# Optimization experiments

Measured on AMD Instinct MI355X. Metric: run time of the kernel, lower is better.

## Reference

```python
import jax, jax.numpy as jnp
import numpy as np
from jax import lax

P = 8       # patch_size
TEMP = 30.0 # softmax temperature from RelationUnit.temp


def _conv3x3(x, w, b, groups):
    # x: [B, C, H, W], w: [O, C//groups, 3, 3]
    y = lax.conv_general_dilated(x, w, (1, 1), 'SAME', feature_group_count=groups)
    return y + b[None, :, None, None]


def _unfold(x):
    # nn.Unfold(kernel=P, stride=P): [B,C,H,W] -> [B, C*P*P, n], channel-major then (ki,kj)
    B, C, H, W = x.shape
    x = x.reshape(B, C, H // P, P, W // P, P)
    x = x.transpose(0, 1, 3, 5, 2, 4)          # [B,C,P,P,H/P,W/P]
    return x.reshape(B, C * P * P, (H // P) * (W // P))


def _fold(x, H, W):
    # inverse of _unfold (non-overlapping patches)
    B, CPP, n = x.shape
    C = CPP // (P * P)
    x = x.reshape(B, C, P, P, H // P, W // P)
    x = x.transpose(0, 1, 4, 2, 5, 3)          # [B,C,H/P,P,W/P,P]
    return x.reshape(B, C, H, W)


def _head(query, key, value, wq, bq, wk, bk, wv, bv):
    # one RelationUnit (heads=1 internally)
    b, tq, c, h, w = query.shape
    t = key.shape[1]
    n = (h // P) * (w // P)
    d = P * P * c

    q = _conv3x3(query.reshape(-1, c, h, w), wq, bq, groups=c)   # depthwise
    k = _conv3x3(key.reshape(-1, c, h, w), wk, bk, groups=c)     # depthwise
    v = _conv3x3(value.reshape(-1, c, h, w), wv, bv, groups=1)   # dense

    # [b*t, d, n] -> [b, d, t*n]  (matches view/permute chain in torch code)
    uq = _unfold(q).reshape(b, tq, d, n).transpose(0, 2, 1, 3).reshape(b, d, tq * n)
    uk = _unfold(k).reshape(b, t, d, n).transpose(0, 2, 1, 3).reshape(b, d, t * n)
    uv = _unfold(v).reshape(b, t, d, n).transpose(0, 2, 1, 3).reshape(b, d, t * n)

    attn = jnp.einsum('bdq,bdk->bqk', uq, uk) * (d ** -0.5)
    attn = jax.nn.softmax(attn * TEMP, axis=-1)
    out = jnp.einsum('bqk,bdk->bqd', attn, uv)                   # [b, tq*n, d]

    out = out.reshape(b, tq, n, d).transpose(0, 1, 3, 2).reshape(b * tq, d, n)
    feat = _fold(out, h, w)                                      # [b*tq, c, h, w]
    return feat.reshape(query.shape)


def reference(query, key, value, Wq, bq, Wk, bk, Wv, bv):
    heads = jax.vmap(_head, in_axes=(None, None, None, 0, 0, 0, 0, 0, 0))(
        query, key, value, Wq, bq, Wk, bk, Wv, bv)               # [Nh, b, tq, c, h, w]
    Nh = heads.shape[0]
    return jnp.concatenate([heads[i] for i in range(Nh)], axis=-1)


def setup_inputs() -> dict:
    key = jax.random.key(0)
    ks = jax.random.split(key, 6)
    b, tq, t, c, h, w, Nh = 1, 2, 2, 32, 224, 336, 4
    f32 = jnp.float32
    rn = lambda k, s, sc=1.0: jax.random.normal(k, s, f32) * sc
    return {
        'query': rn(ks[0], (b, tq, c, h, w)),
        'key':   rn(ks[1], (b, t, c, h, w)),
        'value': rn(ks[2], (b, t, c, h, w)),
        'Wq': rn(ks[3], (Nh, c, 1, 3, 3), 0.1), 'bq': jnp.zeros((Nh, c), f32),
        'Wk': rn(ks[4], (Nh, c, 1, 3, 3), 0.1), 'bk': jnp.zeros((Nh, c), f32),
        'Wv': rn(ks[5], (Nh, c, c, 3, 3), 0.05), 'bv': jnp.zeros((Nh, c), f32),
    }
```

## Files before the change

kernel.cpp:

```cpp
#include <hip/hip_runtime.h>
#include <hip/hip_bf16.h>

#define T_FR 2
#define C_CH 32
#define H_IMG 224
#define W_IMG 336
#define NH 4
#define NPATCH 1176
#define NQ 2352
#define NPAD 2432
#define DD 2048
#define WOUT (W_IMG*NH)
#define SM_SCALE 0.6629126073623885f
#define PIX_F (H_IMG*W_IMG)
#define PIX_T (T_FR*PIX_F)

typedef __attribute__((ext_vector_type(4))) float f32x4;
typedef __attribute__((ext_vector_type(8))) short short8;
typedef unsigned short ushort_t;
typedef __attribute__((ext_vector_type(4))) unsigned short u16x4;
typedef __attribute__((ext_vector_type(8))) unsigned short u16x8;

__device__ inline ushort_t f2bf(float x){
  union { float f; unsigned int u; } v; v.f = x;
  unsigned int r = v.u + 0x7fffu + ((v.u >> 16) & 1u);
  return (ushort_t)(r >> 16);
}

__device__ inline void gload16(const void* g, void* l){
  __builtin_amdgcn_global_load_lds(
      (const __attribute__((address_space(1))) void*)g,
      (__attribute__((address_space(3))) void*)l,
      16, 0, 0);
}

__global__ __launch_bounds__(256) void zero_pads(
    ushort_t* __restrict__ Qu, ushort_t* __restrict__ Ku,
    ushort_t* __restrict__ Vu, int nh)
{
  const int per = 80*DD;
  int tot = 3*nh*per;
  for (int id = blockIdx.x*256 + threadIdx.x; id < tot; id += gridDim.x*256){
    int buf = id / (nh*per);
    int rem = id - buf*(nh*per);
    int h = rem / per;
    int e = rem - h*per;
    ushort_t* B = (buf==0) ? Qu : (buf==1) ? Ku : Vu;
    B[((size_t)h*NPAD + NQ)*DD + e] = 0;
  }
}

__global__ __launch_bounds__(256) void transpose_cl(
    const float* __restrict__ in, ushort_t* __restrict__ inCL)
{
  int id = blockIdx.x*256 + threadIdx.x;
  int t = id / PIX_F;
  int p = id - t*PIX_F;
  const float* src = in + (size_t)t*C_CH*PIX_F + p;
  #pragma unroll
  for (int oct=0; oct<4; oct++){
    u16x8 u;
    #pragma unroll
    for (int e=0; e<8; e++)
      u[e] = f2bf(src[(size_t)(oct*8+e)*PIX_F]);
    *(u16x8*)&inCL[(size_t)id*C_CH + oct*8] = u;
  }
}

__global__ __launch_bounds__(256) void prep_wb(
    const float* __restrict__ Wv, ushort_t* __restrict__ Wb)
{
  int idx = blockIdx.x*256 + threadIdx.x;
  if (idx >= 9*128*32) return;
  int tap = idx >> 12;
  int og  = (idx >> 5) & 127;
  int cc  = idx & 31;
  Wb[idx] = f2bf(Wv[(size_t)og*288 + cc*9 + tap]);
}

__global__ __launch_bounds__(256) void dwconv_unfold(
    const float* __restrict__ in, const float* __restrict__ Wd,
    const float* __restrict__ bd, ushort_t* __restrict__ outU,
    int head0, int nh)
{
  int id = blockIdx.x*256 + threadIdx.x;
  int cc = id & 31;
  int rest = id >> 5;
  int xseg = rest % 42;
  rest /= 42;
  int y = rest % H_IMG;
  int t = rest / H_IMG;

  const float* src = in + ((size_t)(t*C_CH + cc)*H_IMG)*W_IMG;
  int x0 = xseg*8;

  float r0[10], r1[10], r2[10];
  #pragma unroll
  for (int j=0;j<10;j++){
    int xx = x0 + j - 1;
    bool xok = (xx>=0) && (xx<W_IMG);
    r0[j] = (xok && y>0)         ? src[(size_t)(y-1)*W_IMG+xx] : 0.f;
    r1[j] = (xok)                ? src[(size_t)y*W_IMG+xx]     : 0.f;
    r2[j] = (xok && y<H_IMG-1)   ? src[(size_t)(y+1)*W_IMG+xx] : 0.f;
  }
  int qrow = t*NPATCH + (y>>3)*42 + xseg;
  int dcol = (y&7)*256 + cc*8;

  for (int h = 0; h < nh; ++h){
    const float* w = Wd + ((size_t)(head0+h)*C_CH + cc)*9;
    float w0=w[0],w1=w[1],w2=w[2],w3=w[3],w4=w[4],w5=w[5],w6=w[6],w7=w[7],w8=w[8];
    float bias = bd[(size_t)(head0+h)*C_CH + cc];
    u16x8 res;
    #pragma unroll
    for (int j=0;j<8;j++){
      float a = bias;
      a += r0[j]*w0 + r0[j+1]*w1 + r0[j+2]*w2;
      a += r1[j]*w3 + r1[j+1]*w4 + r1[j+2]*w5;
      a += r2[j]*w6 + r2[j+1]*w7 + r2[j+2]*w8;
      res[j] = f2bf(a);
    }
    *(u16x8*)&outU[((size_t)h*NPAD + qrow)*DD + dcol] = res;
  }
}

#define VA_HALO 0
#define VA_BS   37120
#define V_LDS   73984

__global__ __launch_bounds__(256) void vconv_mfma(
    const ushort_t* __restrict__ inCL, const ushort_t* __restrict__ Wb,
    const float* __restrict__ bvv, ushort_t* __restrict__ Vu, int head0)
{
  __shared__ __align__(16) char lds[V_LDS];
  int xt = blockIdx.x;
  int pr_g = blockIdx.y;
  int z  = blockIdx.z;
  int t  = pr_g / 28, pr = pr_g - t*28;
  int x0 = xt*56, y0 = pr*8;
  int tid = threadIdx.x, lane = tid & 63, wid = tid >> 6;

  for (int i = tid; i < 580; i += 256){
    int ly = i/58, lx = i - (i/58)*58;
    int gy = y0 - 1 + ly, gx = x0 - 1 + lx;
    u16x8 v0={},v1={},v2={},v3={};
    if (gy>=0 && gy<H_IMG && gx>=0 && gx<W_IMG){
      const u16x8* s = (const u16x8*)&inCL[((size_t)t*PIX_F + gy*W_IMG + gx)*C_CH];
      v0=s[0]; v1=s[1]; v2=s[2]; v3=s[3];
    }
    *(u16x8*)&lds[VA_HALO + 0*9280 + i*16] = v0;
    *(u16x8*)&lds[VA_HALO + 1*9280 + i*16] = v1;
    *(u16x8*)&lds[VA_HALO + 2*9280 + i*16] = v2;
    *(u16x8*)&lds[VA_HALO + 3*9280 + i*16] = v3;
  }
  for (int i = tid; i < 576; i += 256){
    int tap = i/64, ol = i - (i/64)*64;
    const u16x8* s = (const u16x8*)&Wb[((size_t)tap*128 + head0*32 + z*64 + ol)*C_CH];
    #pragma unroll
    for (int oct=0; oct<4; oct++)
      *(u16x8*)&lds[VA_BS + tap*4096 + ol*64 + ((oct^(ol&3))<<4)] = s[oct];
  }
  __syncthreads();

  int aoff[7];
  #pragma unroll
  for (int m=0;m<7;m++){
    int pm = wid*112 + m*16 + (lane&15);
    int yl = pm/56, xl = pm - yl*56;
    aoff[m] = VA_HALO + (lane>>4)*9280 + (yl*58 + xl)*16;
  }

  f32x4 acc[7][4] = {};
  #pragma unroll
  for (int tap=0; tap<9; tap++){
    const int dy = tap/3, dx = tap - (tap/3)*3;
    short8 bfr[4];
    #pragma unroll
    for (int n=0;n<4;n++){
      int ol = n*16 + (lane&15);
      bfr[n] = *(const short8*)&lds[VA_BS + tap*4096 + ol*64 + ((((lane>>4))^(ol&3))<<4)];
    }
    #pragma unroll
    for (int m=0;m<7;m++){
      short8 af = *(const short8*)&lds[aoff[m] + (dy*58+dx)*16];
      #pragma unroll
      for (int n=0;n<4;n++)
        acc[m][n] = __builtin_amdgcn_mfma_f32_16x16x32_bf16(af, bfr[n], acc[m][n], 0,0,0);
    }
  }
  __syncthreads();

  float bias[4];
  #pragma unroll
  for (int n=0;n<4;n++){
    int ol = n*16 + (lane&15);
    bias[n] = bvv[(size_t)(head0 + z*2 + (ol>>5))*C_CH + (ol&31)];
  }
  #pragma unroll
  for (int m=0;m<7;m++){
    #pragma unroll
    for (int j=0;j<4;j++){
      int p = wid*112 + m*16 + (lane>>4)*4 + j;
      int yl = p/56, xl = p - (p/56)*56;
      int kl = xl >> 3;
      int off = yl*8 + (xl&7);
      #pragma unroll
      for (int n=0;n<4;n++){
        int ol = n*16 + (lane&15);
        int addr = ((ol>>5)*7 + kl)*4096 + (off*32 + (ol&31))*2;
        *(ushort_t*)&lds[addr] = f2bf(acc[m][n][j] + bias[n]);
      }
    }
  }
  __syncthreads();
  int key0 = t*NPATCH + pr*42 + xt*7;
  #pragma unroll
  for (int i=0;i<14;i++){
    int c = i*256 + tid;
    int hib = c / 1792;
    int rem = c - hib*1792;
    int kl = rem >> 8, dch = rem & 255;
    u16x8 v = *(const u16x8*)&lds[c*16];
    *(u16x8*)&Vu[((size_t)(z*2+hib)*NPAD + key0 + kl)*DD + dch*8] = v;
  }
}

__global__ __launch_bounds__(256) void vtranspose(
    const ushort_t* __restrict__ Vu, ushort_t* __restrict__ Vt)
{
  __shared__ ushort_t tile[64*68];
  int d0 = blockIdx.x*64;
  int k0 = blockIdx.y*64;
  const ushort_t* src = Vu + (size_t)blockIdx.z*NPAD*DD;
  ushort_t* dst = Vt + (size_t)blockIdx.z*DD*NPAD;
  int t = threadIdx.x;
  #pragma unroll
  for (int i=0;i<2;i++){
    int key = (t>>3) + i*32;
    int dd  = (t&7)*8;
    u16x8 v = *(const u16x8*)&src[(size_t)(k0+key)*DD + d0+dd];
    #pragma unroll
    for (int e=0;e<8;e++) tile[(dd+e)*68 + key] = v[e];
  }
  __syncthreads();
  #pragma unroll
  for (int i=0;i<2;i++){
    int dd  = (t>>3) + i*32;
    int key = (t&7)*8;
    u16x4 a = *(const u16x4*)&tile[dd*68 + key];
    u16x4 b = *(const u16x4*)&tile[dd*68 + key + 4];
    u16x8 v;
    v[0]=a[0]; v[1]=a[1]; v[2]=a[2]; v[3]=a[3];
    v[4]=b[0]; v[5]=b[1]; v[6]=b[2]; v[7]=b[3];
    *(u16x8*)&dst[(size_t)(d0+dd)*NPAD + k0+key] = v;
  }
}

#define ABASE(b,kc) ((b)*32768 + (kc)*16384)
#define BBASE(b,kc) (65536 + (b)*32768 + (kc)*16384)

#define STG(dstb, Mat, t0, Rm1, ktc) { \
  int i0_ = tid;       int r0_ = i0_>>2; int c0_ = ((i0_&3) ^ ((r0_>>1)&3)); \
  gload16(Mat + (size_t)min(t0 + r0_, Rm1)*(size_t)K + (ktc) + c0_*8, \
          lds + (dstb) + (tid & ~63)*16); \
  int i1_ = 512 + tid; int r1_ = i1_>>2; int c1_ = ((i1_&3) ^ ((r1_>>1)&3)); \
  gload16(Mat + (size_t)min(t0 + r1_, Rm1)*(size_t)K + (ktc) + c1_*8, \
          lds + (dstb) + (512 + (tid & ~63))*16); }

#define RDAF(b,kc,mh) { _Pragma("unroll") \
  for (int m=0;m<4;m++) \
    af[m] = *(const short8*)(lds + ABASE(b,kc) + (wr*128 + (mh)*64 + m*16 + l15)*64 + rkB); }

#define RDBF(b,kc) { _Pragma("unroll") \
  for (int n=0;n<4;n++) \
    bf[n] = *(const short8*)(lds + BBASE(b,kc) + (wc*64 + n*16 + l15)*64 + rkB); }

#define LEADBAR() { __builtin_amdgcn_sched_barrier(0); \
  __builtin_amdgcn_s_barrier(); __builtin_amdgcn_sched_barrier(0); }

#define MFMA16(mh) { __builtin_amdgcn_s_setprio(1); \
  _Pragma("unroll") for (int m=0;m<4;m++){ \
    _Pragma("unroll") for (int n=0;n<4;n++) \
      acc[(mh)*4+m][n] = __builtin_amdgcn_mfma_f32_16x16x32_bf16(af[m], bf[n], acc[(mh)*4+m][n], 0,0,0); } \
  __builtin_amdgcn_s_setprio(0); }

#define TRAILBAR() { __builtin_amdgcn_sched_barrier(0); \
  __builtin_amdgcn_s_barrier(); __builtin_amdgcn_sched_barrier(0); }

#define GATEBAR(cond) { __builtin_amdgcn_sched_barrier(0); \
  if (cond) { asm volatile("s_waitcnt vmcnt(4)" ::: "memory"); } \
  else      { asm volatile("s_waitcnt vmcnt(0)" ::: "memory"); } \
  __builtin_amdgcn_s_barrier(); __builtin_amdgcn_sched_barrier(0); }

template<int MODE>
__global__ __launch_bounds__(512) void gemm8p(
    const ushort_t* __restrict__ A, const ushort_t* __restrict__ B,
    float* __restrict__ C, float* __restrict__ Out,
    int K, int Am1, int Bm1, size_t aStr, size_t bStr, int head0)
{
  __shared__ __align__(16) char lds[131072];
  int tid = threadIdx.x, lane = tid & 63, wid = tid >> 6;

  int gx = gridDim.x, gy = gridDim.y;
  int nwg = gx*gy*gridDim.z;
  int id  = (blockIdx.z*gy + blockIdx.y)*gx + blockIdx.x;
  int swz = (id & 7)*(nwg >> 3) + (id >> 3);
  int bx = swz % gx; int tmp = swz / gx;
  int by = tmp % gy; int bz = tmp / gy;

  const ushort_t* Ab = A + (size_t)bz*aStr;
  const ushort_t* Bb = B + (size_t)bz*bStr;
  int row0 = by*256, col0 = bx*256;
  int wr = wid >> 2, wc = wid & 3;
  int l15 = lane & 15;
  int rkB = (((lane>>4) ^ ((l15>>1)&3)) * 16);

  f32x4 acc[8][4] = {};
  int NT = K >> 6;
  int NI = NT >> 1;

  STG(ABASE(0,0), Ab, row0, Am1, 0)
  STG(BBASE(0,0), Bb, col0, Bm1, 0)
  STG(ABASE(0,1), Ab, row0, Am1, 32)
  STG(BBASE(0,1), Bb, col0, Bm1, 32)
  STG(ABASE(1,0), Ab, row0, Am1, 64)
  STG(BBASE(1,0), Bb, col0, Bm1, 64)
  __builtin_amdgcn_sched_barrier(0);
  asm volatile("s_waitcnt vmcnt(4)" ::: "memory");
  __builtin_amdgcn_s_barrier();
  __builtin_amdgcn_sched_barrier(0);

  #pragma unroll 1
  for (int it = 0; it < NI; ++it){
    int T1k = (2*it+1) << 6;
    int T2k = (2*it+2) << 6;
    int T3k = (2*it+3) << 6;
    bool s2 = (2*it+2 < NT), s3 = (2*it+3 < NT);
    short8 af[4], bf[4];

    RDAF(0,0,0) RDBF(0,0)
    STG(ABASE(1,1), Ab, row0, Am1, T1k+32)
    LEADBAR() MFMA16(0) TRAILBAR()
    RDAF(0,0,1)
    STG(BBASE(1,1), Bb, col0, Bm1, T1k+32)
    LEADBAR() MFMA16(1) TRAILBAR()
    RDAF(0,1,0) RDBF(0,1)
    if (s2) STG(ABASE(0,0), Ab, row0, Am1, T2k)
    LEADBAR() MFMA16(0) TRAILBAR()
    RDAF(0,1,1)
    if (s2) STG(BBASE(0,0), Bb, col0, Bm1, T2k)
    LEADBAR() MFMA16(1)
    GATEBAR(s2)
    RDAF(1,0,0) RDBF(1,0)
    if (s2) STG(ABASE(0,1), Ab, row0, Am1, T2k+32)
    LEADBAR() MFMA16(0) TRAILBAR()
    RDAF(1,0,1)
    if (s2) STG(BBASE(0,1), Bb, col0, Bm1, T2k+32)
    LEADBAR() MFMA16(1) TRAILBAR()
    RDAF(1,1,0) RDBF(1,1)
    if (s3) STG(ABASE(1,0), Ab, row0, Am1, T3k)
    LEADBAR() MFMA16(0) TRAILBAR()
    RDAF(1,1,1)
    if (s3) STG(BBASE(1,0), Bb, col0, Bm1, T3k)
    LEADBAR() MFMA16(1)
    GATEBAR(s3)
  }

  int rb0 = row0 + wr*128 + (lane>>4)*4;
  int cb0 = col0 + wc*64 + l15;
  if (MODE == 0){
    float* Cb = C + (size_t)bz*NPAD*(size_t)NPAD;
    #pragma unroll
    for (int M=0;M<8;M++)
      #pragma unroll
      for (int n=0;n<4;n++){
        int col = cb0 + n*16;
        if (col < NPAD)
          #pragma unroll
          for (int j=0;j<4;j++){
            int row = rb0 + M*16 + j;
            if (row < NPAD)
              Cb[(size_t)row*NPAD + col] = acc[M][n][j];
          }
      }
  } else {
    int head = head0 + bz;
    #pragma unroll
    for (int M=0;M<8;M++){
      #pragma unroll
      for (int j=0;j<4;j++){
        int q = rb0 + M*16 + j;
        if (q < NQ){
          int t = q / NPATCH;
          int p = q - t*NPATCH;
          int hi = p / 42, wi = p - hi*42;
          #pragma unroll
          for (int n=0;n<4;n++){
            int dd = cb0 + n*16;
            int cch = dd & 31;
            int off = dd >> 5;
            int pi = off >> 3, pj = off & 7;
            int yy = hi*8 + pi, xx = wi*8 + pj;
            Out[(((size_t)t*C_CH + cch)*H_IMG + yy)*WOUT + (size_t)head*W_IMG + xx]
              = acc[M][n][j];
          }
        }
      }
    }
  }
}

__global__ __launch_bounds__(256) void softmax_rows(
    const float* __restrict__ S, ushort_t* __restrict__ Pm)
{
  const float* row = S + ((size_t)blockIdx.y*NPAD + blockIdx.x)*NPAD;
  ushort_t* prow = Pm + ((size_t)blockIdx.y*NPAD + blockIdx.x)*NPAD;
  int tid = threadIdx.x;
  __shared__ float red[4];

  float mx = -3.0e38f;
  #pragma unroll
  for (int i=0;i<10;i++){
    int k = tid + i*256;
    if (k < NQ) mx = fmaxf(mx, row[k]);
  }
  #pragma unroll
  for (int o=32;o;o>>=1) mx = fmaxf(mx, __shfl_xor(mx, o));
  if ((tid&63)==0) red[tid>>6] = mx;
  __syncthreads();
  mx = fmaxf(fmaxf(red[0],red[1]), fmaxf(red[2],red[3]));
  __syncthreads();

  float e[10]; float s = 0.f;
  #pragma unroll
  for (int i=0;i<10;i++){
    int k = tid + i*256;
    float v = 0.f;
    if (k < NQ) v = __expf((row[k]-mx)*SM_SCALE);
    e[i] = v; s += v;
  }
  #pragma unroll
  for (int o=32;o;o>>=1) s += __shfl_xor(s, o);
  if ((tid&63)==0) red[tid>>6] = s;
  __syncthreads();
  s = (red[0]+red[1]) + (red[2]+red[3]);
  float inv = 1.0f / s;
  #pragma unroll
  for (int i=0;i<10;i++){
    int k = tid + i*256;
    if (k < NQ) prow[k] = f2bf(e[i]*inv);
  }
  if (tid < NPAD-NQ) prow[NQ+tid] = 0;
}

extern "C" void kernel_launch(void* const* d_in, const int* in_sizes, int n_in,
                              void* d_out, int out_size, void* d_ws, size_t ws_size,
                              hipStream_t stream)
{
  const float* query = (const float*)d_in[0];
  const float* key_  = (const float*)d_in[1];
  const float* value = (const float*)d_in[2];
  const float* Wq = (const float*)d_in[3];
  const float* bq = (const float*)d_in[4];
  const float* Wk = (const float*)d_in[5];
  const float* bk = (const float*)d_in[6];
  const float* Wv = (const float*)d_in[7];
  const float* bv = (const float*)d_in[8];
  float* out = (float*)d_out;

  const size_t szU = (size_t)NPAD*DD;
  const size_t szS = (size_t)NPAD*NPAD;
  const size_t perHeadB = 3*szU*sizeof(ushort_t) + szS*sizeof(float) + szS*sizeof(ushort_t);

  int nh = (ws_size >= 4*perHeadB) ? 4 : 2;

  for (int h0 = 0; h0 < NH; h0 += nh){
    char* p = (char*)d_ws;
    ushort_t* Qu = (ushort_t*)p; p += nh*szU*sizeof(ushort_t);
    ushort_t* Ku = (ushort_t*)p; p += nh*szU*sizeof(ushort_t);
    ushort_t* Vu = (ushort_t*)p; p += nh*szU*sizeof(ushort_t);
    float*    S  = (float*)p;    p += nh*szS*sizeof(float);
    ushort_t* Pm = (ushort_t*)p;
    ushort_t* inCL = (ushort_t*)S;
    ushort_t* Wb   = inCL + (size_t)PIX_T*C_CH;
    ushort_t* Vt   = Qu;

    zero_pads<<<dim3(960), dim3(256), 0, stream>>>(Qu, Ku, Vu, nh);
    transpose_cl<<<dim3(588), dim3(256), 0, stream>>>(value, inCL);
    prep_wb<<<dim3(144), dim3(256), 0, stream>>>(Wv, Wb);
    dwconv_unfold<<<dim3(2352), dim3(256), 0, stream>>>(query, Wq, bq, Qu, h0, nh);
    dwconv_unfold<<<dim3(2352), dim3(256), 0, stream>>>(key_,  Wk, bk, Ku, h0, nh);
    vconv_mfma<<<dim3(6, 56, nh/2), dim3(256), 0, stream>>>(inCL, Wb, bv, Vu, h0);
    gemm8p<0><<<dim3(10, 10, nh), dim3(512), 0, stream>>>(
        Qu, Ku, S, nullptr, DD, NPAD-1, NPAD-1, szU, szU, h0);
    vtranspose<<<dim3(32, 38, nh), dim3(256), 0, stream>>>(Vu, Vt);
    softmax_rows<<<dim3(NPAD, nh), dim3(256), 0, stream>>>(S, Pm);
    gemm8p<1><<<dim3(8, 10, nh), dim3(512), 0, stream>>>(
        Pm, Vt, nullptr, out, NPAD, NPAD-1, DD-1, szS, szU, h0);
  }
}
```

Measured before the change: 486.4 us.

## Double-buffer LDS fragment reads in registers to overlap with MFMA in GEMM

Restructures the bf16 GEMM main loop so the A/B fragments for the next MFMA phase are read from LDS into a second register set while the current phase's MFMAs run. This replaces the lead/trail barrier pair around each phase with a single barrier per phase, and uses a fixed vmcnt(2) gate instead of the conditional vmcnt. The first fragments are prefetched before the loop, and there is a full drain after it. It costs extra VGPRs for the second fragment set, which may reduce occupancy or cause spills. The reworked barrier and waitcnt placement also carries correctness risk at the loop boundaries.

```diff
diff --git a/kernel.cpp b/kernel.cpp
--- a/kernel.cpp
+++ b/kernel.cpp
@@ -266,29 +266,25 @@
   gload16(Mat + (size_t)min(t0 + r1_, Rm1)*(size_t)K + (ktc) + c1_*8, \
           lds + (dstb) + (512 + (tid & ~63))*16); }
 
-#define RDAF(b,kc,mh) { _Pragma("unroll") \
+#define RD_A(dst, b, kc, mh) { _Pragma("unroll") \
   for (int m=0;m<4;m++) \
-    af[m] = *(const short8*)(lds + ABASE(b,kc) + (wr*128 + (mh)*64 + m*16 + l15)*64 + rkB); }
-
-#define RDBF(b,kc) { _Pragma("unroll") \
+    dst[m] = *(const short8*)(lds + ABASE(b,kc) + (wr*128 + (mh)*64 + m*16 + l15)*64 + rkB); }
+
+#define RD_B(dst, b, kc) { _Pragma("unroll") \
   for (int n=0;n<4;n++) \
-    bf[n] = *(const short8*)(lds + BBASE(b,kc) + (wc*64 + n*16 + l15)*64 + rkB); }
-
-#define LEADBAR() { __builtin_amdgcn_sched_barrier(0); \
-  __builtin_amdgcn_s_barrier(); __builtin_amdgcn_sched_barrier(0); }
-
-#define MFMA16(mh) { __builtin_amdgcn_s_setprio(1); \
+    dst[n] = *(const short8*)(lds + BBASE(b,kc) + (wc*64 + n*16 + l15)*64 + rkB); }
+
+#define DO_MFMA(afS, bfS, mh) { __builtin_amdgcn_s_setprio(1); \
   _Pragma("unroll") for (int m=0;m<4;m++){ \
     _Pragma("unroll") for (int n=0;n<4;n++) \
-      acc[(mh)*4+m][n] = __builtin_amdgcn_mfma_f32_16x16x32_bf16(af[m], bf[n], acc[(mh)*4+m][n], 0,0,0); } \
+      acc[(mh)*4+m][n] = __builtin_amdgcn_mfma_f32_16x16x32_bf16(afS[m], bfS[n], acc[(mh)*4+m][n], 0,0,0); } \
   __builtin_amdgcn_s_setprio(0); }
 
-#define TRAILBAR() { __builtin_amdgcn_sched_barrier(0); \
+#define BAR() { __builtin_amdgcn_sched_barrier(0); \
   __builtin_amdgcn_s_barrier(); __builtin_amdgcn_sched_barrier(0); }
 
-#define GATEBAR(cond) { __builtin_amdgcn_sched_barrier(0); \
-  if (cond) { asm volatile("s_waitcnt vmcnt(4)" ::: "memory"); } \
-  else      { asm volatile("s_waitcnt vmcnt(0)" ::: "memory"); } \
+#define GATE2() { __builtin_amdgcn_sched_barrier(0); \
+  asm volatile("s_waitcnt vmcnt(2)" ::: "memory"); \
   __builtin_amdgcn_s_barrier(); __builtin_amdgcn_sched_barrier(0); }
 
 template<int MODE>
@@ -317,6 +313,8 @@
   f32x4 acc[8][4] = {};
   int NT = K >> 6;
   int NI = NT >> 1;
+
+  short8 af0[4], af1[4], bf0[4], bf1[4];
 
   STG(ABASE(0,0), Ab, row0, Am1, 0)
   STG(BBASE(0,0), Bb, col0, Bm1, 0)
@@ -328,42 +326,51 @@
   asm volatile("s_waitcnt vmcnt(4)" ::: "memory");
   __builtin_amdgcn_s_barrier();
   __builtin_amdgcn_sched_barrier(0);
+  RD_A(af0, 0,0,0) RD_B(bf0, 0,0)
 
   #pragma unroll 1
   for (int it = 0; it < NI; ++it){
     int T1k = (2*it+1) << 6;
     int T2k = (2*it+2) << 6;
     int T3k = (2*it+3) << 6;
-    bool s2 = (2*it+2 < NT), s3 = (2*it+3 < NT);
-    short8 af[4], bf[4];
-
-    RDAF(0,0,0) RDBF(0,0)
+    bool s2ok = (2*it+2 < NT), s3ok = (2*it+3 < NT);
+
+    BAR()
     STG(ABASE(1,1), Ab, row0, Am1, T1k+32)
-    LEADBAR() MFMA16(0) TRAILBAR()
-    RDAF(0,0,1)
+    RD_A(af1, 0,0,1)
+    DO_MFMA(af0, bf0, 0)
+    BAR()
     STG(BBASE(1,1), Bb, col0, Bm1, T1k+32)
-    LEADBAR() MFMA16(1) TRAILBAR()
-    RDAF(0,1,0) RDBF(0,1)
-    if (s2) STG(ABASE(0,0), Ab, row0, Am1, T2k)
-    LEADBAR() MFMA16(0) TRAILBAR()
-    RDAF(0,1,1)
-    if (s2) STG(BBASE(0,0), Bb, col0, Bm1, T2k)
-    LEADBAR() MFMA16(1)
-    GATEBAR(s2)
-    RDAF(1,0,0) RDBF(1,0)
-    if (s2) STG(ABASE(0,1), Ab, row0, Am1, T2k+32)
-    LEADBAR() MFMA16(0) TRAILBAR()
-    RDAF(1,0,1)
-    if (s2) STG(BBASE(0,1), Bb, col0, Bm1, T2k+32)
-    LEADBAR() MFMA16(1) TRAILBAR()
-    RDAF(1,1,0) RDBF(1,1)
-    if (s3) STG(ABASE(1,0), Ab, row0, Am1, T3k)
-    LEADBAR() MFMA16(0) TRAILBAR()
-    RDAF(1,1,1)
-    if (s3) STG(BBASE(1,0), Bb, col0, Bm1, T3k)
-    LEADBAR() MFMA16(1)
-    GATEBAR(s3)
-  }
+    RD_A(af0, 0,1,0) RD_B(bf1, 0,1)
+    DO_MFMA(af1, bf0, 1)
+    BAR()
+    if (s2ok) STG(ABASE(0,0), Ab, row0, Am1, T2k)
+    RD_A(af1, 0,1,1)
+    DO_MFMA(af0, bf1, 0)
+    GATE2()
+    if (s2ok) STG(BBASE(0,0), Bb, col0, Bm1, T2k)
+    RD_A(af0, 1,0,0) RD_B(bf0, 1,0)
+    DO_MFMA(af1, bf1, 1)
+    BAR()
+    if (s2ok) STG(ABASE(0,1), Ab, row0, Am1, T2k+32)
+    RD_A(af1, 1,0,1)
+    DO_MFMA(af0, bf0, 0)
+    BAR()
+    if (s2ok) STG(BBASE(0,1), Bb, col0, Bm1, T2k+32)
+    RD_A(af0, 1,1,0) RD_B(bf1, 1,1)
+    DO_MFMA(af1, bf0, 1)
+    BAR()
+    if (s3ok) STG(ABASE(1,0), Ab, row0, Am1, T3k)
+    RD_A(af1, 1,1,1)
+    DO_MFMA(af0, bf1, 0)
+    GATE2()
+    if (s3ok) STG(BBASE(1,0), Bb, col0, Bm1, T3k)
+    RD_A(af0, 0,0,0) RD_B(bf0, 0,0)
+    DO_MFMA(af1, bf1, 1)
+  }
+  __builtin_amdgcn_sched_barrier(0);
+  asm volatile("s_waitcnt vmcnt(0) lgkmcnt(0)" ::: "memory");
+  __builtin_amdgcn_sched_barrier(0);
 
   int rb0 = row0 + wr*128 + (lane>>4)*4;
   int cb0 = col0 + wc*64 + l15;
```

New measurement: 550.1 us. +13.1%, slower.
